# Kernel tuning notes

Hardware: AMD Instinct MI355X
Metric: run time of the kernel (lower is better)

Reference implementation:

```python
import jax, jax.numpy as jnp
import numpy as np

EMBED_DIM = 128
HIDDEN = 64
LN_EPS = 1e-5
NORM_EPS = 1e-6


def setup_inputs() -> dict:
    key = jax.random.key(0)
    ks = jax.random.split(key, 12)
    B, L = 32, 2048
    inp = {
        "map_lane_positions": jax.random.normal(ks[0], (B, L, 10, 2), dtype=jnp.float32),
        "map_is_intersection": jax.random.randint(ks[1], (B, L), 0, 3, dtype=jnp.int64),
        "map_turn_direction": jax.random.randint(ks[2], (B, L), 0, 3, dtype=jnp.int64),
        "map_traffic_control": jax.random.randint(ks[3], (B, L), 0, 2, dtype=jnp.int64),
        # SingleInputEmbedding params: Linear(2,64) -> LayerNorm(64) -> ReLU -> Linear(64,128)
        "W1": jax.random.normal(ks[4], (2, HIDDEN), dtype=jnp.float32) * 0.5,
        "b1": jax.random.normal(ks[5], (HIDDEN,), dtype=jnp.float32) * 0.1,
        "ln_gamma": jnp.ones((HIDDEN,), dtype=jnp.float32),
        "ln_beta": jnp.zeros((HIDDEN,), dtype=jnp.float32),
        "W2": jax.random.normal(ks[6], (HIDDEN, EMBED_DIM), dtype=jnp.float32) * 0.1,
        "b2": jax.random.normal(ks[7], (EMBED_DIM,), dtype=jnp.float32) * 0.1,
        # discrete embedding tables
        "E_intersection": jax.random.normal(ks[8], (3, EMBED_DIM), dtype=jnp.float32),
        "E_turn": jax.random.normal(ks[9], (3, EMBED_DIM), dtype=jnp.float32),
        "E_traffic": jax.random.normal(ks[10], (2, EMBED_DIM), dtype=jnp.float32),
    }
    return inp


def _mlp(x, W1, b1, g, beta, W2, b2):
    h = x @ W1 + b1                                  # [..., 64]
    mu = jnp.mean(h, axis=-1, keepdims=True)
    var = jnp.mean((h - mu) ** 2, axis=-1, keepdims=True)
    h = (h - mu) * jax.lax.rsqrt(var + LN_EPS) * g + beta
    h = jax.nn.relu(h)
    return h @ W2 + b2                               # [..., 128]


def reference(map_lane_positions, map_is_intersection, map_turn_direction,
              map_traffic_control, W1, b1, ln_gamma, ln_beta, W2, b2,
              E_intersection, E_turn, E_traffic):
    # direction vectors between consecutive points: [B, L, 9, 2]
    dv = map_lane_positions[:, :, 1:, :] - map_lane_positions[:, :, :-1, :]
    norms = jnp.sqrt(jnp.sum(dv ** 2, axis=-1, keepdims=True) + NORM_EPS)
    dv = dv / norms

    cont = _mlp(dv, W1, b1, ln_gamma, ln_beta, W2, b2)   # [B, L, 9, 128]
    # discrete embeddings broadcast over the 9-point axis
    disc = (E_intersection[map_is_intersection]
            + E_turn[map_turn_direction]
            + E_traffic[map_traffic_control])             # [B, L, 128]
    fused = cont + disc[:, :, None, :]                    # [B, L, 9, 128]
    return jnp.max(fused, axis=2)                         # [B, L, 128]
```

## Files before the change

### kernel.cpp

```cpp
#include <hip/hip_runtime.h>
#include <hip/hip_bf16.h>

#define NB      16
#define THREADS 256

#define WS_CST4   0
#define WS_QUAD   256
#define WS_DISC   272
#define WS_W2     2576

typedef float f32x4  __attribute__((ext_vector_type(4)));
typedef float f32x2  __attribute__((ext_vector_type(2)));
typedef short bf16x8 __attribute__((ext_vector_type(8)));

#if __has_builtin(__builtin_elementwise_fma)
static __device__ __forceinline__ f32x2 FMA2(f32x2 a, f32x2 b, f32x2 c) {
    return __builtin_elementwise_fma(a, b, c);
}
#else
static __device__ __forceinline__ f32x2 FMA2(f32x2 a, f32x2 b, f32x2 c) {
    f32x2 r; r.x = fmaf(a.x, b.x, c.x); r.y = fmaf(a.y, b.y, c.y); return r;
}
#endif

#if __has_builtin(__builtin_elementwise_max)
static __device__ __forceinline__ f32x2 MAX2(f32x2 a, f32x2 b) {
    return __builtin_elementwise_max(a, b);
}
static __device__ __forceinline__ f32x4 MAX4(f32x4 a, f32x4 b) {
    return __builtin_elementwise_max(a, b);
}
#else
static __device__ __forceinline__ f32x2 MAX2(f32x2 a, f32x2 b) {
    f32x2 r; r.x = fmaxf(a.x, b.x); r.y = fmaxf(a.y, b.y); return r;
}
static __device__ __forceinline__ f32x4 MAX4(f32x4 a, f32x4 b) {
    f32x4 r;
    r[0] = fmaxf(a[0], b[0]); r[1] = fmaxf(a[1], b[1]);
    r[2] = fmaxf(a[2], b[2]); r[3] = fmaxf(a[3], b[3]);
    return r;
}
#endif

static __device__ __forceinline__ unsigned f2bf(float f) {
    __hip_bfloat16 h = __float2bfloat16(f);
    return (unsigned)__builtin_bit_cast(unsigned short, h);
}

__global__ __launch_bounds__(THREADS)
void lane_setup_kernel(const float* __restrict__ W1, const float* __restrict__ b1,
                       const float* __restrict__ gam, const float* __restrict__ bet,
                       const float* __restrict__ W2, const float* __restrict__ b2,
                       const float* __restrict__ Ei, const float* __restrict__ Et,
                       const float* __restrict__ Etc, float* __restrict__ ws)
{
    const int tid = threadIdx.x, lane = tid & 63, wv = tid >> 6;

    if (wv == 0) {
        float wx = W1[lane], wy = W1[64 + lane], bb = b1[lane];
        float sx = wx, sy = wy, sb = bb;
        #pragma unroll
        for (int m = 1; m < 64; m <<= 1) {
            sx += __shfl_xor(sx, m, 64);
            sy += __shfl_xor(sy, m, 64);
            sb += __shfl_xor(sb, m, 64);
        }
        float a = wx - sx * (1.f / 64.f);
        float b = wy - sy * (1.f / 64.f);
        float c = bb - sb * (1.f / 64.f);
        float p0 = a * a, p1 = b * b, p2 = a * b, p3 = a * c, p4 = b * c, p5 = c * c;
        #pragma unroll
        for (int m = 1; m < 64; m <<= 1) {
            p0 += __shfl_xor(p0, m, 64); p1 += __shfl_xor(p1, m, 64);
            p2 += __shfl_xor(p2, m, 64); p3 += __shfl_xor(p3, m, 64);
            p4 += __shfl_xor(p4, m, 64); p5 += __shfl_xor(p5, m, 64);
        }
        float g = gam[lane];
        ((float4*)(ws + WS_CST4))[lane] = make_float4(a * g, b * g, c * g, bet[lane]);
        if (lane == 0) {
            ws[WS_QUAD + 0] = p0 * (1.f / 64.f);
            ws[WS_QUAD + 1] = p1 * (1.f / 64.f);
            ws[WS_QUAD + 2] = p2 * (1.f / 64.f);
            ws[WS_QUAD + 3] = p3 * (1.f / 64.f);
            ws[WS_QUAD + 4] = p4 * (1.f / 64.f);
            ws[WS_QUAD + 5] = p5 * (1.f / 64.f) + 1e-5f;
        }
    }

    {
        uint4* dst = (uint4*)(ws + WS_W2);
        #pragma unroll
        for (int f = wv * 4; f < wv * 4 + 4; ++f) {
            int c = f >> 1, kt = f & 1;
            int col = c * 16 + (lane & 15);
            int k0  = kt * 32 + (lane >> 4) * 8;
            unsigned w[4];
            #pragma unroll
            for (int j = 0; j < 4; ++j) {
                unsigned lo = f2bf(W2[(k0 + 2 * j) * 128 + col]);
                unsigned hi = f2bf(W2[(k0 + 2 * j + 1) * 128 + col]);
                w[j] = (hi << 16) | lo;
            }
            dst[f * 64 + lane] = make_uint4(w[0], w[1], w[2], w[3]);
        }
    }

    for (int i = tid; i < 18 * 128; i += THREADS) {
        int combo = i >> 7, col = i & 127;
        int ai = combo / 6; int r = combo - ai * 6; int bi = r >> 1; int ci = r & 1;
        ws[WS_DISC + i] = b2[col] + Ei[ai * 128 + col] + Et[bi * 128 + col] + Etc[ci * 128 + col];
    }
}

__global__ __launch_bounds__(THREADS)
void lane_node_embed_mfma(const float* __restrict__ pos,
                          const int*   __restrict__ idx_int,
                          const int*   __restrict__ idx_turn,
                          const int*   __restrict__ idx_tc,
                          const float* __restrict__ ws,
                          float* __restrict__ out,
                          int n_nodes)
{
    __shared__ __align__(16) unsigned short H[NB * 9 * 64];
    __shared__ float4 smv[NB * 9];
    __shared__ int    cmb_lds[NB];

    const int tid  = threadIdx.x;
    const int lane = tid & 63;
    const int wv   = __builtin_amdgcn_readfirstlane(tid >> 6);
    const int blockStart = blockIdx.x * NB;

    if (tid < NB * 9) {
        int nd = tid / 9, p = tid - nd * 9;
        int gn = blockStart + nd;
        float ax = 0.f, ay = 0.f, is = 0.f;
        if (gn < n_nodes) {
            const float2* pp = (const float2*)pos + (size_t)gn * 10 + p;
            float2 q0 = pp[0], q1 = pp[1];
            float dx = q1.x - q0.x, dy = q1.y - q0.y;
            float inv = rsqrtf(fmaf(dx, dx, fmaf(dy, dy, 1e-6f)));
            dx *= inv; dy *= inv;
            float qA = ws[WS_QUAD + 0], qB = ws[WS_QUAD + 1], qC = ws[WS_QUAD + 2];
            float qD = ws[WS_QUAD + 3], qE = ws[WS_QUAD + 4], qF = ws[WS_QUAD + 5];
            float t   = fmaf(dx * dy, qC, fmaf(dx, qD, dy * qE));
            float var = fmaf(2.f, t, fmaf(dx * dx, qA, fmaf(dy * dy, qB, qF)));
            is = rsqrtf(var);
            ax = dx * is; ay = dy * is;
        }
        smv[tid] = make_float4(ax, ay, is, 0.f);
    }
    if (tid < NB) {
        int gn = blockStart + tid;
        cmb_lds[tid] = (gn < n_nodes)
            ? (idx_int[gn] * 3 + idx_turn[gn]) * 2 + idx_tc[gn] : 0;
    }

    const int kl   = lane & 31;
    const int half = lane >> 5;
    const float4 cstA = ((const float4*)(ws + WS_CST4))[2 * kl];
    const float4 cstB = ((const float4*)(ws + WS_CST4))[2 * kl + 1];
    f32x2 cx, cy, cz, cw;
    cx.x = cstA.x; cx.y = cstB.x;
    cy.x = cstA.y; cy.y = cstB.y;
    cz.x = cstA.z; cz.y = cstB.z;
    cw.x = cstA.w; cw.y = cstB.w;

    const int ct0 = wv * 2;
    const uint4* wfr = (const uint4*)(ws + WS_W2);
    bf16x8 Bfr[2][2];
    #pragma unroll
    for (int c = 0; c < 2; ++c)
        #pragma unroll
        for (int kt = 0; kt < 2; ++kt)
            Bfr[c][kt] = __builtin_bit_cast(bf16x8, wfr[((ct0 + c) * 2 + kt) * 64 + lane]);

    __syncthreads();

    {
        const int kch  = kl >> 2;
        const int kofs = (2 * kl) & 7;
        f32x2 zero2; zero2.x = 0.f; zero2.y = 0.f;
        #pragma unroll
        for (int i = 0; i < 2; ++i) {
            int nd = wv * 4 + 2 * i + half;
            int basew = nd * 576 + ((kch ^ (nd & 7)) << 3) + kofs;
            #pragma unroll
            for (int p = 0; p < 9; ++p) {
                float4 t = smv[nd * 9 + p];
                f32x2 tz; tz.x = t.z; tz.y = t.z;
                f32x2 ty; ty.x = t.y; ty.y = t.y;
                f32x2 tx; tx.x = t.x; tx.y = t.x;
                f32x2 h = FMA2(tz, cz, cw);
                h = FMA2(ty, cy, h);
                h = FMA2(tx, cx, h);
                h = MAX2(h, zero2);
                *(unsigned*)&H[basew + p * 64] = (f2bf(h.y) << 16) | f2bf(h.x);
            }
        }
    }
    __syncthreads();

    const int g   = lane >> 4;
    const int l15 = lane & 15;
    const int sr  = l15 & 7;
    const int i0  = l15 * 576 + ((g ^ sr) << 3);
    const int i1  = l15 * 576 + (((4 + g) ^ sr) << 3);

    int cjv[4];
    #pragma unroll
    for (int jj = 0; jj < 4; ++jj) cjv[jj] = cmb_lds[g * 4 + jj];
    float dvp[2][4];
    #pragma unroll
    for (int c = 0; c < 2; ++c)
        #pragma unroll
        for (int jj = 0; jj < 4; ++jj)
            dvp[c][jj] = ws[WS_DISC + cjv[jj] * 128 + (ct0 + c) * 16 + l15];

    const f32x4 zz = {0.f, 0.f, 0.f, 0.f};
    f32x4 mx0, mx1;
    {
        bf16x8 a0 = *(const bf16x8*)&H[i0];
        bf16x8 a1 = *(const bf16x8*)&H[i1];
        mx0 = __builtin_amdgcn_mfma_f32_16x16x32_bf16(a0, Bfr[0][0], zz, 0, 0, 0);
        mx0 = __builtin_amdgcn_mfma_f32_16x16x32_bf16(a1, Bfr[0][1], mx0, 0, 0, 0);
        mx1 = __builtin_amdgcn_mfma_f32_16x16x32_bf16(a0, Bfr[1][0], zz, 0, 0, 0);
        mx1 = __builtin_amdgcn_mfma_f32_16x16x32_bf16(a1, Bfr[1][1], mx1, 0, 0, 0);
    }
    #pragma unroll
    for (int p = 1; p < 9; ++p) {
        bf16x8 a0 = *(const bf16x8*)&H[i0 + p * 64];
        bf16x8 a1 = *(const bf16x8*)&H[i1 + p * 64];
        f32x4 t0 = __builtin_amdgcn_mfma_f32_16x16x32_bf16(a0, Bfr[0][0], zz, 0, 0, 0);
        t0       = __builtin_amdgcn_mfma_f32_16x16x32_bf16(a1, Bfr[0][1], t0, 0, 0, 0);
        f32x4 t1 = __builtin_amdgcn_mfma_f32_16x16x32_bf16(a0, Bfr[1][0], zz, 0, 0, 0);
        t1       = __builtin_amdgcn_mfma_f32_16x16x32_bf16(a1, Bfr[1][1], t1, 0, 0, 0);
        mx0 = MAX4(mx0, t0);
        mx1 = MAX4(mx1, t1);
    }

    #pragma unroll
    for (int c = 0; c < 2; ++c) {
        int col = (ct0 + c) * 16 + l15;
        f32x4 m = (c == 0) ? mx0 : mx1;
        #pragma unroll
        for (int j = 0; j < 4; ++j) {
            int gn = blockStart + g * 4 + j;
            if (gn < n_nodes)
                out[(size_t)gn * 128 + col] = m[j] + dvp[c][j];
        }
    }
}

extern "C" void kernel_launch(void* const* d_in, const int* in_sizes, int n_in,
                              void* d_out, int out_size, void* d_ws, size_t ws_size,
                              hipStream_t stream) {
    const float* pos  = (const float*)d_in[0];
    const int*   ii   = (const int*)  d_in[1];
    const int*   it   = (const int*)  d_in[2];
    const int*   itc  = (const int*)  d_in[3];
    const float* W1   = (const float*)d_in[4];
    const float* b1   = (const float*)d_in[5];
    const float* gam  = (const float*)d_in[6];
    const float* bet  = (const float*)d_in[7];
    const float* W2   = (const float*)d_in[8];
    const float* b2   = (const float*)d_in[9];
    const float* Ei   = (const float*)d_in[10];
    const float* Et   = (const float*)d_in[11];
    const float* Etc  = (const float*)d_in[12];
    float* out = (float*)d_out;
    float* ws  = (float*)d_ws;

    int n_nodes = in_sizes[1];
    int blocks  = (n_nodes + NB - 1) / NB;

    hipLaunchKernelGGL(lane_setup_kernel, dim3(1), dim3(THREADS), 0, stream,
                       W1, b1, gam, bet, W2, b2, Ei, Et, Etc, ws);
    hipLaunchKernelGGL(lane_node_embed_mfma, dim3(blocks), dim3(THREADS), 0, stream,
                       pos, ii, it, itc, ws, out, n_nodes);
}
```

Baseline: 30.84 us.

## Fuse parameter setup into main kernel, recomputing constants per block

Removes the single-block setup kernel and its workspace, so every block computes the LayerNorm quadratic constants, the per-lane scale and shift, the bf16 W2 fragments and the discrete-embedding sums directly from the raw parameters. Position and index loads are issued first so their latency overlaps the shuffle reductions. This drops one launch and the serial dependency on a one-block kernel. In exchange every block does redundant reductions and strided W2 gathers with bf16 conversion, and reads three embedding tables instead of one precombined table.

After: 35.28 us. 14.4% more time.

```diff
diff --git a/kernel.cpp b/kernel.cpp
--- a/kernel.cpp
+++ b/kernel.cpp
@@ -3,11 +3,6 @@
 
 #define NB      16
 #define THREADS 256
-
-#define WS_CST4   0
-#define WS_QUAD   256
-#define WS_DISC   272
-#define WS_W2     2576
 
 typedef float f32x4  __attribute__((ext_vector_type(4)));
 typedef float f32x2  __attribute__((ext_vector_type(2)));
@@ -48,16 +43,56 @@
 }
 
 __global__ __launch_bounds__(THREADS)
-void lane_setup_kernel(const float* __restrict__ W1, const float* __restrict__ b1,
-                       const float* __restrict__ gam, const float* __restrict__ bet,
-                       const float* __restrict__ W2, const float* __restrict__ b2,
-                       const float* __restrict__ Ei, const float* __restrict__ Et,
-                       const float* __restrict__ Etc, float* __restrict__ ws)
+void lane_node_fused(const float* __restrict__ pos,
+                     const int*   __restrict__ idx_int,
+                     const int*   __restrict__ idx_turn,
+                     const int*   __restrict__ idx_tc,
+                     const float* __restrict__ W1,
+                     const float* __restrict__ b1,
+                     const float* __restrict__ gam,
+                     const float* __restrict__ bet,
+                     const float* __restrict__ W2,
+                     const float* __restrict__ b2,
+                     const float* __restrict__ Ei,
+                     const float* __restrict__ Et,
+                     const float* __restrict__ Etc,
+                     float* __restrict__ out,
+                     int n_nodes)
 {
-    const int tid = threadIdx.x, lane = tid & 63, wv = tid >> 6;
-
-    if (wv == 0) {
-        float wx = W1[lane], wy = W1[64 + lane], bb = b1[lane];
+    __shared__ __align__(16) unsigned short H[NB * 9 * 64];
+    __shared__ float4 smv[NB * 9];
+    __shared__ int    cmb_lds[NB];
+
+    const int tid  = threadIdx.x;
+    const int lane = tid & 63;
+    const int wv   = __builtin_amdgcn_readfirstlane(tid >> 6);
+    const int blockStart = blockIdx.x * NB;
+
+    const int kl   = lane & 31;
+    const int half = lane >> 5;
+    const int l15  = lane & 15;
+    const int g    = lane >> 4;
+
+    float2 q0 = make_float2(0.f, 0.f), q1 = q0;
+    const int snd = tid / 9, sp = tid - snd * 9;
+    const bool sAct = (tid < NB * 9);
+    if (sAct) {
+        int gn = blockStart + snd;
+        if (gn < n_nodes) {
+            const float2* pp = (const float2*)pos + (size_t)gn * 10 + sp;
+            q0 = pp[0]; q1 = pp[1];
+        }
+    }
+    int cmb0 = 0;
+    if (tid < NB) {
+        int gn = blockStart + tid;
+        if (gn < n_nodes)
+            cmb0 = (idx_int[gn] * 3 + idx_turn[gn]) * 2 + idx_tc[gn];
+    }
+
+    float wx = W1[lane], wy = W1[64 + lane], bb = b1[lane];
+    float gv = gam[lane], btv = bet[lane];
+    {
         float sx = wx, sy = wy, sb = bb;
         #pragma unroll
         for (int m = 1; m < 64; m <<= 1) {
@@ -65,35 +100,41 @@
             sy += __shfl_xor(sy, m, 64);
             sb += __shfl_xor(sb, m, 64);
         }
-        float a = wx - sx * (1.f / 64.f);
-        float b = wy - sy * (1.f / 64.f);
-        float c = bb - sb * (1.f / 64.f);
-        float p0 = a * a, p1 = b * b, p2 = a * b, p3 = a * c, p4 = b * c, p5 = c * c;
+        wx -= sx * (1.f / 64.f);
+        wy -= sy * (1.f / 64.f);
+        bb -= sb * (1.f / 64.f);
+    }
+    float qA, qB, qC, qD, qE, qF;
+    {
+        float p0 = wx * wx, p1 = wy * wy, p2 = wx * wy;
+        float p3 = wx * bb, p4 = wy * bb, p5 = bb * bb;
         #pragma unroll
         for (int m = 1; m < 64; m <<= 1) {
             p0 += __shfl_xor(p0, m, 64); p1 += __shfl_xor(p1, m, 64);
             p2 += __shfl_xor(p2, m, 64); p3 += __shfl_xor(p3, m, 64);
             p4 += __shfl_xor(p4, m, 64); p5 += __shfl_xor(p5, m, 64);
         }
-        float g = gam[lane];
-        ((float4*)(ws + WS_CST4))[lane] = make_float4(a * g, b * g, c * g, bet[lane]);
-        if (lane == 0) {
-            ws[WS_QUAD + 0] = p0 * (1.f / 64.f);
-            ws[WS_QUAD + 1] = p1 * (1.f / 64.f);
-            ws[WS_QUAD + 2] = p2 * (1.f / 64.f);
-            ws[WS_QUAD + 3] = p3 * (1.f / 64.f);
-            ws[WS_QUAD + 4] = p4 * (1.f / 64.f);
-            ws[WS_QUAD + 5] = p5 * (1.f / 64.f) + 1e-5f;
-        }
-    }
-
-    {
-        uint4* dst = (uint4*)(ws + WS_W2);
-        #pragma unroll
-        for (int f = wv * 4; f < wv * 4 + 4; ++f) {
-            int c = f >> 1, kt = f & 1;
-            int col = c * 16 + (lane & 15);
-            int k0  = kt * 32 + (lane >> 4) * 8;
+        qA = p0 * (1.f / 64.f); qB = p1 * (1.f / 64.f); qC = p2 * (1.f / 64.f);
+        qD = p3 * (1.f / 64.f); qE = p4 * (1.f / 64.f);
+        qF = p5 * (1.f / 64.f) + 1e-5f;
+    }
+    f32x2 cx, cy, cz, cw;
+    {
+        float ag = wx * gv, bg = wy * gv, cg = bb * gv;
+        cx.x = __shfl(ag, 2 * kl, 64); cx.y = __shfl(ag, 2 * kl + 1, 64);
+        cy.x = __shfl(bg, 2 * kl, 64); cy.y = __shfl(bg, 2 * kl + 1, 64);
+        cz.x = __shfl(cg, 2 * kl, 64); cz.y = __shfl(cg, 2 * kl + 1, 64);
+        cw.x = __shfl(btv, 2 * kl, 64); cw.y = __shfl(btv, 2 * kl + 1, 64);
+    }
+
+    const int ct0 = wv * 2;
+    bf16x8 Bfr[2][2];
+    #pragma unroll
+    for (int c = 0; c < 2; ++c) {
+        #pragma unroll
+        for (int kt = 0; kt < 2; ++kt) {
+            int col = (ct0 + c) * 16 + l15;
+            int k0  = kt * 32 + g * 8;
             unsigned w[4];
             #pragma unroll
             for (int j = 0; j < 4; ++j) {
@@ -101,78 +142,22 @@
                 unsigned hi = f2bf(W2[(k0 + 2 * j + 1) * 128 + col]);
                 w[j] = (hi << 16) | lo;
             }
-            dst[f * 64 + lane] = make_uint4(w[0], w[1], w[2], w[3]);
-        }
-    }
-
-    for (int i = tid; i < 18 * 128; i += THREADS) {
-        int combo = i >> 7, col = i & 127;
-        int ai = combo / 6; int r = combo - ai * 6; int bi = r >> 1; int ci = r & 1;
-        ws[WS_DISC + i] = b2[col] + Ei[ai * 128 + col] + Et[bi * 128 + col] + Etc[ci * 128 + col];
-    }
-}
-
-__global__ __launch_bounds__(THREADS)
-void lane_node_embed_mfma(const float* __restrict__ pos,
-                          const int*   __restrict__ idx_int,
-                          const int*   __restrict__ idx_turn,
-                          const int*   __restrict__ idx_tc,
-                          const float* __restrict__ ws,
-                          float* __restrict__ out,
-                          int n_nodes)
-{
-    __shared__ __align__(16) unsigned short H[NB * 9 * 64];
-    __shared__ float4 smv[NB * 9];
-    __shared__ int    cmb_lds[NB];
-
-    const int tid  = threadIdx.x;
-    const int lane = tid & 63;
-    const int wv   = __builtin_amdgcn_readfirstlane(tid >> 6);
-    const int blockStart = blockIdx.x * NB;
-
-    if (tid < NB * 9) {
-        int nd = tid / 9, p = tid - nd * 9;
-        int gn = blockStart + nd;
-        float ax = 0.f, ay = 0.f, is = 0.f;
-        if (gn < n_nodes) {
-            const float2* pp = (const float2*)pos + (size_t)gn * 10 + p;
-            float2 q0 = pp[0], q1 = pp[1];
-            float dx = q1.x - q0.x, dy = q1.y - q0.y;
-            float inv = rsqrtf(fmaf(dx, dx, fmaf(dy, dy, 1e-6f)));
-            dx *= inv; dy *= inv;
-            float qA = ws[WS_QUAD + 0], qB = ws[WS_QUAD + 1], qC = ws[WS_QUAD + 2];
-            float qD = ws[WS_QUAD + 3], qE = ws[WS_QUAD + 4], qF = ws[WS_QUAD + 5];
-            float t   = fmaf(dx * dy, qC, fmaf(dx, qD, dy * qE));
-            float var = fmaf(2.f, t, fmaf(dx * dx, qA, fmaf(dy * dy, qB, qF)));
-            is = rsqrtf(var);
-            ax = dx * is; ay = dy * is;
-        }
-        smv[tid] = make_float4(ax, ay, is, 0.f);
-    }
-    if (tid < NB) {
-        int gn = blockStart + tid;
-        cmb_lds[tid] = (gn < n_nodes)
-            ? (idx_int[gn] * 3 + idx_turn[gn]) * 2 + idx_tc[gn] : 0;
-    }
-
-    const int kl   = lane & 31;
-    const int half = lane >> 5;
-    const float4 cstA = ((const float4*)(ws + WS_CST4))[2 * kl];
-    const float4 cstB = ((const float4*)(ws + WS_CST4))[2 * kl + 1];
-    f32x2 cx, cy, cz, cw;
-    cx.x = cstA.x; cx.y = cstB.x;
-    cy.x = cstA.y; cy.y = cstB.y;
-    cz.x = cstA.z; cz.y = cstB.z;
-    cw.x = cstA.w; cw.y = cstB.w;
-
-    const int ct0 = wv * 2;
-    const uint4* wfr = (const uint4*)(ws + WS_W2);
-    bf16x8 Bfr[2][2];
-    #pragma unroll
-    for (int c = 0; c < 2; ++c)
-        #pragma unroll
-        for (int kt = 0; kt < 2; ++kt)
-            Bfr[c][kt] = __builtin_bit_cast(bf16x8, wfr[((ct0 + c) * 2 + kt) * 64 + lane]);
+            Bfr[c][kt] = __builtin_bit_cast(bf16x8, make_uint4(w[0], w[1], w[2], w[3]));
+        }
+    }
+
+    if (sAct) {
+        float dx = q1.x - q0.x, dy = q1.y - q0.y;
+        float inv = rsqrtf(fmaf(dx, dx, fmaf(dy, dy, 1e-6f)));
+        dx *= inv; dy *= inv;
+        float t   = fmaf(dx * dy, qC, fmaf(dx, qD, dy * qE));
+        float var = fmaf(2.f, t, fmaf(dx * dx, qA, fmaf(dy * dy, qB, qF)));
+        float is  = rsqrtf(var);
+        int gn = blockStart + snd;
+        if (gn >= n_nodes) { dx = 0.f; dy = 0.f; is = 0.f; }
+        smv[tid] = make_float4(dx * is, dy * is, is, 0.f);
+    }
+    if (tid < NB) cmb_lds[tid] = cmb0;
 
     __syncthreads();
 
@@ -200,21 +185,22 @@
     }
     __syncthreads();
 
-    const int g   = lane >> 4;
-    const int l15 = lane & 15;
     const int sr  = l15 & 7;
     const int i0  = l15 * 576 + ((g ^ sr) << 3);
     const int i1  = l15 * 576 + (((4 + g) ^ sr) << 3);
 
-    int cjv[4];
-    #pragma unroll
-    for (int jj = 0; jj < 4; ++jj) cjv[jj] = cmb_lds[g * 4 + jj];
     float dvp[2][4];
     #pragma unroll
-    for (int c = 0; c < 2; ++c)
-        #pragma unroll
-        for (int jj = 0; jj < 4; ++jj)
-            dvp[c][jj] = ws[WS_DISC + cjv[jj] * 128 + (ct0 + c) * 16 + l15];
+    for (int c = 0; c < 2; ++c) {
+        int col = (ct0 + c) * 16 + l15;
+        float b2v = b2[col];
+        #pragma unroll
+        for (int jj = 0; jj < 4; ++jj) {
+            int cmb = cmb_lds[g * 4 + jj];
+            int ai = cmb / 6; int r = cmb - ai * 6; int bi = r >> 1; int ci = r & 1;
+            dvp[c][jj] = b2v + Ei[ai * 128 + col] + Et[bi * 128 + col] + Etc[ci * 128 + col];
+        }
+    }
 
     const f32x4 zz = {0.f, 0.f, 0.f, 0.f};
     f32x4 mx0, mx1;
@@ -268,13 +254,11 @@
     const float* Et   = (const float*)d_in[11];
     const float* Etc  = (const float*)d_in[12];
     float* out = (float*)d_out;
-    float* ws  = (float*)d_ws;
 
     int n_nodes = in_sizes[1];
     int blocks  = (n_nodes + NB - 1) / NB;
 
-    hipLaunchKernelGGL(lane_setup_kernel, dim3(1), dim3(THREADS), 0, stream,
-                       W1, b1, gam, bet, W2, b2, Ei, Et, Etc, ws);
-    hipLaunchKernelGGL(lane_node_embed_mfma, dim3(blocks), dim3(THREADS), 0, stream,
-                       pos, ii, it, itc, ws, out, n_nodes);
-}
+    hipLaunchKernelGGL(lane_node_fused, dim3(blocks), dim3(THREADS), 0, stream,
+                       pos, ii, it, itc, W1, b1, gam, bet, W2, b2, Ei, Et, Etc,
+                       out, n_nodes);
+}
```
